# Kernel optimization log

Measured on AMD Instinct MI355X. Metric: run time of the kernel, lower is better.

Reference implementation:

```python
import jax, jax.numpy as jnp
import numpy as np

EMBED_DIM = 2048
NUM_HEADS = 32
NUM_KV_HEADS = 8
HEAD_DIM = EMBED_DIM // NUM_HEADS  # 64
KV_DIM = NUM_KV_HEADS * HEAD_DIM   # 512


def setup_inputs() -> dict:
    key = jax.random.key(0)
    ks = jax.random.split(key, 5)
    B, S = 2, 2048
    scale = 0.02
    x = jax.random.normal(ks[0], (B, S, EMBED_DIM), dtype=jnp.float32)
    Wq = jax.random.normal(ks[1], (EMBED_DIM, EMBED_DIM), dtype=jnp.float32) * scale
    Wk = jax.random.normal(ks[2], (EMBED_DIM, KV_DIM), dtype=jnp.float32) * scale
    Wv = jax.random.normal(ks[3], (EMBED_DIM, KV_DIM), dtype=jnp.float32) * scale
    Wo = jax.random.normal(ks[4], (EMBED_DIM, EMBED_DIM), dtype=jnp.float32) * scale
    return {"x": x, "Wq": Wq, "Wk": Wk, "Wv": Wv, "Wo": Wo}


def reference(x, Wq, Wk, Wv, Wo):
    B, S, _ = x.shape
    g = NUM_HEADS // NUM_KV_HEADS  # queries per kv head
    # projections -> [B, H, S, D]
    q = (x @ Wq).reshape(B, S, NUM_HEADS, HEAD_DIM).transpose(0, 2, 1, 3)
    k = (x @ Wk).reshape(B, S, NUM_KV_HEADS, HEAD_DIM).transpose(0, 2, 1, 3)
    v = (x @ Wv).reshape(B, S, NUM_KV_HEADS, HEAD_DIM).transpose(0, 2, 1, 3)
    # GQA repeat_interleave on head dim
    k = jnp.repeat(k, g, axis=1)
    v = jnp.repeat(v, g, axis=1)
    scores = jnp.einsum('bhqd,bhkd->bhqk', q, k) / np.sqrt(HEAD_DIM).astype(np.float32)
    causal = jnp.tril(jnp.ones((S, S), dtype=bool))
    scores = jnp.where(causal, scores, jnp.finfo(x.dtype).min)
    attn = jax.nn.softmax(scores, axis=-1)
    out = jnp.einsum('bhqk,bhkd->bhqd', attn, v)  # [B, H, S, D]
    out = out.transpose(0, 2, 1, 3).reshape(B, S, EMBED_DIM)
    return out @ Wo
```

## Files before the change

### kernel.cpp

```cpp
#include <hip/hip_runtime.h>
#include <hip/hip_bf16.h>
#include <cstdint>
#include <type_traits>

#define EMBED 2048
#define SLEN 2048
#define NB 2
#define NHEADS 32
#define HDIM 64
#define KVDIM 512
#define KVSTRIDE 1024
#define MTOT (NB * SLEN)
#define NQKV (EMBED + 2 * KVDIM)

typedef __attribute__((ext_vector_type(8))) __bf16 bf16x8;
typedef __attribute__((ext_vector_type(4))) float f32x4;
typedef __attribute__((ext_vector_type(16))) float f32x16;

#define QSCALE 0.18033688011112042f

__device__ __forceinline__ ushort f2bf(float f) {
    union { float f; uint32_t u; } v; v.f = f;
    uint32_t r = (v.u + 0x7FFFu + ((v.u >> 16) & 1u)) >> 16;
    return (ushort)r;
}

__device__ __forceinline__ void gload_lds16(const ushort* g, ushort* l) {
    __builtin_amdgcn_global_load_lds(
        (const __attribute__((address_space(1))) void*)g,
        (__attribute__((address_space(3))) void*)l, 16, 0, 0);
}

__global__ __launch_bounds__(256) void k_prep(const float* __restrict__ x,
                                              const float* __restrict__ Wq,
                                              const float* __restrict__ Wk,
                                              const float* __restrict__ Wv,
                                              const float* __restrict__ Wo,
                                              ushort* __restrict__ xb,
                                              ushort* __restrict__ wt,
                                              ushort* __restrict__ wot) {
    const int tid = threadIdx.x;
    int bid = blockIdx.x;
    if (bid < 8192) {
        int i = bid * 256 + tid;
        float4 v = *(const float4*)(x + (size_t)i * 4);
        ushort4 o;
        o.x = f2bf(v.x); o.y = f2bf(v.y); o.z = f2bf(v.z); o.w = f2bf(v.w);
        *(ushort4*)(xb + (size_t)i * 4) = o;
        return;
    }
    bid -= 8192;
    const float* W; ushort* Wt; int N; float scale; int bx, by;
    if (bid < 4096)      { W = Wq; Wt = wt;                                   N = EMBED; scale = QSCALE; bx = bid & 63; by = bid >> 6; }
    else if (bid < 5120) { W = Wk; Wt = wt + (size_t)EMBED * EMBED;           N = KVDIM; scale = 1.f; int b2 = bid - 4096; bx = b2 & 15; by = b2 >> 4; }
    else if (bid < 6144) { W = Wv; Wt = wt + (size_t)(EMBED + KVDIM) * EMBED; N = KVDIM; scale = 1.f; int b2 = bid - 5120; bx = b2 & 15; by = b2 >> 4; }
    else                 { W = Wo; Wt = wot;                                  N = EMBED; scale = 1.f; int b2 = bid - 6144; bx = b2 & 63; by = b2 >> 6; }
    const int K = EMBED;
    __shared__ float tile[32][33];
    const int tx = tid & 31, ty = tid >> 5;
    const int xcol = bx * 32 + tx;
    const int y0 = by * 32;
    #pragma unroll
    for (int i = ty; i < 32; i += 8)
        tile[i][tx] = W[(size_t)(y0 + i) * N + xcol];
    __syncthreads();
    const int xo = y0 + tx;
    const int yo0 = bx * 32;
    #pragma unroll
    for (int i = ty; i < 32; i += 8)
        Wt[(size_t)(yo0 + i) * K + xo] = f2bf(tile[tx][i] * scale);
}

__global__ __launch_bounds__(256) void k_transpose_v(const ushort* __restrict__ KV,
                                                     ushort* __restrict__ VT) {
    __shared__ ushort tile[64][65];
    const int tx = threadIdx.x, ty = threadIdx.y;
    const int x0 = blockIdx.x * 64;
    const int y0 = blockIdx.y * 64;
    #pragma unroll
    for (int i = ty; i < 64; i += 4)
        tile[i][tx] = KV[(size_t)(y0 + i) * KVSTRIDE + KVDIM + x0 + tx];
    __syncthreads();
    #pragma unroll
    for (int i = ty; i < 64; i += 4)
        VT[(size_t)(x0 + i) * MTOT + y0 + tx] = tile[tx][i];
}

__device__ __forceinline__ int2 xcd_swizzle(int gx, int gy) {
    const int nwg = gx * gy;
    int f = blockIdx.y * gx + blockIdx.x;
    const int cpx = nwg >> 3;
    f = (f & 7) * cpx + (f >> 3);
    return make_int2(f % gx, f / gx);
}

template <typename OUT_T>
__global__ __launch_bounds__(256) void k_gemm_bt(const ushort* __restrict__ A,
                                                 const ushort* __restrict__ Bt,
                                                 OUT_T* __restrict__ C,
                                                 int M, int N, int K) {
    __shared__ alignas(16) ushort As[2][128 * 64];
    __shared__ alignas(16) ushort Bs[2][128 * 64];

    const int tid = threadIdx.x;
    const int lane = tid & 63;
    const int w = tid >> 6;
    const int wr = w >> 1, wc = w & 1;
    const int l15 = lane & 15, g = lane >> 4;
    const int2 bxy = xcd_swizzle(N / 128, M / 128);
    const int n0 = bxy.x * 128;
    const int m0 = bxy.y * 128;

    f32x4 acc[4][4] = {};

    const ushort* pA[4];
    const ushort* pB[4];
    #pragma unroll
    for (int t = 0; t < 4; t++) {
        const int c = tid + 256 * t;
        const int r = c >> 3, gr = c & 7;
        const int sg = gr ^ (r & 7);
        pA[t] = A + (size_t)(m0 + r) * K + sg * 8;
        pB[t] = Bt + (size_t)(n0 + r) * K + sg * 8;
    }

    #pragma unroll
    for (int t = 0; t < 4; t++) {
        gload_lds16(pA[t], &As[0][(tid + 256 * t) * 8]);
        gload_lds16(pB[t], &Bs[0][(tid + 256 * t) * 8]);
    }
    __syncthreads();

    int cur = 0;
    for (int k0 = 0; k0 < K; k0 += 64) {
        if (k0 + 64 < K) {
            #pragma unroll
            for (int t = 0; t < 4; t++) {
                gload_lds16(pA[t] + k0 + 64, &As[cur ^ 1][(tid + 256 * t) * 8]);
                gload_lds16(pB[t] + k0 + 64, &Bs[cur ^ 1][(tid + 256 * t) * 8]);
            }
        }
        #pragma unroll
        for (int kk = 0; kk < 2; kk++) {
            bf16x8 a[4], b[4];
            #pragma unroll
            for (int i = 0; i < 4; i++)
                a[i] = *(const bf16x8*)&As[cur][(wr * 64 + i * 16 + l15) * 64 +
                                                (((4 * kk + g) ^ (l15 & 7)) << 3)];
            #pragma unroll
            for (int j = 0; j < 4; j++)
                b[j] = *(const bf16x8*)&Bs[cur][(wc * 64 + j * 16 + l15) * 64 +
                                                (((4 * kk + g) ^ (l15 & 7)) << 3)];
            #pragma unroll
            for (int i = 0; i < 4; i++)
                #pragma unroll
                for (int j = 0; j < 4; j++)
                    acc[i][j] = __builtin_amdgcn_mfma_f32_16x16x32_bf16(a[i], b[j], acc[i][j], 0, 0, 0);
        }
        __syncthreads();
        cur ^= 1;
    }

    #pragma unroll
    for (int i = 0; i < 4; i++) {
        #pragma unroll
        for (int j = 0; j < 4; j++) {
            const int row = m0 + wr * 64 + i * 16 + g * 4;
            const int col = n0 + wc * 64 + j * 16 + l15;
            #pragma unroll
            for (int r = 0; r < 4; r++) {
                float val = acc[i][j][r];
                if constexpr (std::is_same<OUT_T, ushort>::value)
                    C[(size_t)(row + r) * N + col] = f2bf(val);
                else
                    C[(size_t)(row + r) * N + col] = val;
            }
        }
    }
}

__global__ __launch_bounds__(256) void k_gemm_kv(const ushort* __restrict__ A,
                                                 const ushort* __restrict__ Bt,
                                                 ushort* __restrict__ C) {
    __shared__ alignas(16) ushort As[2][64 * 64];
    __shared__ alignas(16) ushort Bs[2][128 * 64];

    const int tid = threadIdx.x;
    const int lane = tid & 63;
    const int w = tid >> 6;
    const int wr = w >> 1, wc = w & 1;
    const int l15 = lane & 15, g = lane >> 4;
    const int2 bxy = xcd_swizzle(KVSTRIDE / 128, MTOT / 64);
    const int n0 = bxy.x * 128;
    const int m0 = bxy.y * 64;
    const int K = EMBED;

    f32x4 acc[2][4] = {};

    const ushort* pA[2];
    const ushort* pB[4];
    #pragma unroll
    for (int t = 0; t < 2; t++) {
        const int c = tid + 256 * t;
        const int r = c >> 3, gr = c & 7;
        const int sg = gr ^ (r & 7);
        pA[t] = A + (size_t)(m0 + r) * K + sg * 8;
    }
    #pragma unroll
    for (int t = 0; t < 4; t++) {
        const int c = tid + 256 * t;
        const int r = c >> 3, gr = c & 7;
        const int sg = gr ^ (r & 7);
        pB[t] = Bt + (size_t)(n0 + r) * K + sg * 8;
    }

    #pragma unroll
    for (int t = 0; t < 2; t++)
        gload_lds16(pA[t], &As[0][(tid + 256 * t) * 8]);
    #pragma unroll
    for (int t = 0; t < 4; t++)
        gload_lds16(pB[t], &Bs[0][(tid + 256 * t) * 8]);
    __syncthreads();

    int cur = 0;
    for (int k0 = 0; k0 < K; k0 += 64) {
        if (k0 + 64 < K) {
            #pragma unroll
            for (int t = 0; t < 2; t++)
                gload_lds16(pA[t] + k0 + 64, &As[cur ^ 1][(tid + 256 * t) * 8]);
            #pragma unroll
            for (int t = 0; t < 4; t++)
                gload_lds16(pB[t] + k0 + 64, &Bs[cur ^ 1][(tid + 256 * t) * 8]);
        }
        #pragma unroll
        for (int kk = 0; kk < 2; kk++) {
            bf16x8 a[2], b[4];
            #pragma unroll
            for (int i = 0; i < 2; i++)
                a[i] = *(const bf16x8*)&As[cur][(wr * 32 + i * 16 + l15) * 64 +
                                                (((4 * kk + g) ^ (l15 & 7)) << 3)];
            #pragma unroll
            for (int j = 0; j < 4; j++)
                b[j] = *(const bf16x8*)&Bs[cur][(wc * 64 + j * 16 + l15) * 64 +
                                                (((4 * kk + g) ^ (l15 & 7)) << 3)];
            #pragma unroll
            for (int i = 0; i < 2; i++)
                #pragma unroll
                for (int j = 0; j < 4; j++)
                    acc[i][j] = __builtin_amdgcn_mfma_f32_16x16x32_bf16(a[i], b[j], acc[i][j], 0, 0, 0);
        }
        __syncthreads();
        cur ^= 1;
    }

    #pragma unroll
    for (int i = 0; i < 2; i++) {
        #pragma unroll
        for (int j = 0; j < 4; j++) {
            const int row = m0 + wr * 32 + i * 16 + g * 4;
            const int col = n0 + wc * 64 + j * 16 + l15;
            #pragma unroll
            for (int r = 0; r < 4; r++)
                C[(size_t)(row + r) * KVSTRIDE + col] = f2bf(acc[i][j][r]);
        }
    }
}

__global__ __launch_bounds__(512, 4) void k_attn(const ushort* __restrict__ Qg,
                                                 const ushort* __restrict__ KVg,
                                                 const ushort* __restrict__ VTg,
                                                 ushort* __restrict__ Og) {
    __shared__ alignas(16) ushort Ks[2][64 * 64];
    __shared__ alignas(16) ushort Vs[2][64 * 64];

    const int tid = threadIdx.x;
    const int lane = tid & 63;
    const int wq = tid >> 6;
    const int l31 = lane & 31;
    const int hi = lane >> 5;

    const int flat = blockIdx.x + (blockIdx.y << 3) + (blockIdx.z << 8);
    const int lo = flat & 255, hv = flat >> 8;
    const int bi = hv ? (7 - (lo & 7)) : (lo & 7);
    const int h = lo >> 3;
    const int b = hv;
    const int kh = h >> 2;
    const size_t rowbase = (size_t)b * SLEN;

    const int q0 = bi * 256;
    const int qw0 = q0 + wq * 32;
    const int nt = (q0 >> 6) + 4;

    bf16x8 qf[4];
    {
        const ushort* qrow = Qg + (rowbase + qw0 + l31) * EMBED + h * HDIM;
        #pragma unroll
        for (int s = 0; s < 4; s++)
            qf[s] = *(const bf16x8*)(qrow + s * 16 + hi * 8);
    }

    const int srow = tid >> 3;
    const int sgr = tid & 7;
    const int woff = srow * 64 + ((sgr ^ (srow & 7)) << 3);
    const ushort* kgbase = KVg + (rowbase + srow) * KVSTRIDE + kh * HDIM + sgr * 8;
    const ushort* vgbase = VTg + (size_t)(kh * HDIM + srow) * MTOT + b * SLEN + sgr * 8;

    {
        uint4 kr = *(const uint4*)kgbase;
        uint4 vr = *(const uint4*)vgbase;
        *(uint4*)&Ks[0][woff] = kr;
        *(uint4*)&Vs[0][woff] = vr;
    }
    __syncthreads();

    f32x16 oacc[2];
    #pragma unroll
    for (int d = 0; d < 2; d++)
        #pragma unroll
        for (int r = 0; r < 16; r++) oacc[d][r] = 0.f;
    float l_run = 0.f;

    int cur = 0;
    for (int kt = 0; kt < nt; ++kt) {
        const int k0 = kt * 64;
        const bool pref = (kt + 1 < nt);
        uint4 kr, vr;
        if (pref) {
            kr = *(const uint4*)(kgbase + (size_t)(k0 + 64) * KVSTRIDE);
            vr = *(const uint4*)(vgbase + k0 + 64);
        }

        if (k0 <= qw0 + 31) {
            f32x16 sacc[2];
            #pragma unroll
            for (int st = 0; st < 2; st++)
                #pragma unroll
                for (int r = 0; r < 16; r++) sacc[st][r] = 0.f;
            __builtin_amdgcn_s_setprio(1);
            #pragma unroll
            for (int st = 0; st < 2; st++) {
                const int krow = st * 32 + l31;
                #pragma unroll
                for (int s = 0; s < 4; s++) {
                    bf16x8 af = *(const bf16x8*)&Ks[cur][krow * 64 + (((2 * s + hi) ^ (l31 & 7)) << 3)];
                    sacc[st] = __builtin_amdgcn_mfma_f32_32x32x16_bf16(af, qf[s], sacc[st], 0, 0, 0);
                }
            }
            __builtin_amdgcn_s_setprio(0);
            if (k0 + 63 > qw0) {
                const int q = qw0 + l31;
                #pragma unroll
                for (int st = 0; st < 2; st++)
                    #pragma unroll
                    for (int r = 0; r < 16; r++) {
                        int kpos = k0 + st * 32 + (r & 3) + 8 * (r >> 2) + 4 * hi;
                        if (kpos > q) sacc[st][r] = -1e30f;
                    }
            }
            float lsum = 0.f;
            #pragma unroll
            for (int st = 0; st < 2; st++)
                #pragma unroll
                for (int r = 0; r < 16; r++) {
                    float p = __builtin_amdgcn_exp2f(sacc[st][r]);
                    sacc[st][r] = p;
                    lsum += p;
                }
            lsum += __shfl_xor(lsum, 32);
            l_run += lsum;
            uint32_t pr[2][8];
            #pragma unroll
            for (int st = 0; st < 2; st++)
                #pragma unroll
                for (int k = 0; k < 8; k++) {
                    uint32_t d;
                    asm("v_cvt_pk_bf16_f32 %0, %1, %2"
                        : "=v"(d) : "v"(sacc[st][2 * k]), "v"(sacc[st][2 * k + 1]));
                    pr[st][k] = d;
                }
            #pragma unroll
            for (int c = 0; c < 2; c++) {
                #pragma unroll
                for (int tt = 0; tt < 2; tt++) {
                    const int pb = 4 * tt;
                    uint32_t w0 = pr[c][pb + 0], w2 = pr[c][pb + 2];
                    uint32_t w1 = pr[c][pb + 1], w3 = pr[c][pb + 3];
                    asm("v_permlane32_swap_b32 %0, %1" : "+v"(w0), "+v"(w2));
                    asm("v_permlane32_swap_b32 %0, %1" : "+v"(w1), "+v"(w3));
                    union { uint32_t u[4]; bf16x8 v; } pf;
                    pf.u[0] = w0; pf.u[1] = w1; pf.u[2] = w2; pf.u[3] = w3;
                    const int t = 2 * c + tt;
                    __builtin_amdgcn_s_setprio(1);
                    #pragma unroll
                    for (int dt = 0; dt < 2; dt++) {
                        const int vrow = dt * 32 + l31;
                        bf16x8 vf = *(const bf16x8*)&Vs[cur][vrow * 64 + (((2 * t + hi) ^ (l31 & 7)) << 3)];
                        oacc[dt] = __builtin_amdgcn_mfma_f32_32x32x16_bf16(pf.v, vf, oacc[dt], 0, 0, 0);
                    }
                    __builtin_amdgcn_s_setprio(0);
                }
            }
        }

        __syncthreads();
        if (pref) {
            *(uint4*)&Ks[cur ^ 1][woff] = kr;
            *(uint4*)&Vs[cur ^ 1][woff] = vr;
        }
        __syncthreads();
        cur ^= 1;
    }

    #pragma unroll
    for (int r = 0; r < 16; r++) {
        const int rr = (r & 3) + 8 * (r >> 2) + 4 * hi;
        float lr = __shfl(l_run, rr | (lane & 32));
        float inv = 1.f / lr;
        const size_t base = (rowbase + qw0 + rr) * EMBED + h * HDIM;
        Og[base + l31] = f2bf(oacc[0][r] * inv);
        Og[base + 32 + l31] = f2bf(oacc[1][r] * inv);
    }
}

#define WS_XB  ((size_t)0)
#define WS_QB  (WS_XB + (size_t)MTOT * EMBED)
#define WS_KVB (WS_QB + (size_t)MTOT * EMBED)
#define WS_WT  (WS_KVB + (size_t)MTOT * KVSTRIDE)
#define WS_WOT (WS_WT + (size_t)NQKV * EMBED)
#define WS_VT  WS_WT

extern "C" void kernel_launch(void* const* d_in, const int* in_sizes, int n_in,
                              void* d_out, int out_size, void* d_ws, size_t ws_size,
                              hipStream_t stream) {
    const float* x  = (const float*)d_in[0];
    const float* Wq = (const float*)d_in[1];
    const float* Wk = (const float*)d_in[2];
    const float* Wv = (const float*)d_in[3];
    const float* Wo = (const float*)d_in[4];
    float* out = (float*)d_out;
    ushort* ws = (ushort*)d_ws;

    k_prep<<<18432, 256, 0, stream>>>(x, Wq, Wk, Wv, Wo,
                                      ws + WS_XB, ws + WS_WT, ws + WS_WOT);

    k_gemm_bt<ushort><<<dim3(EMBED / 128, MTOT / 128), 256, 0, stream>>>(
        ws + WS_XB, ws + WS_WT, ws + WS_QB, MTOT, EMBED, EMBED);

    k_gemm_kv<<<dim3(KVSTRIDE / 128, MTOT / 64), 256, 0, stream>>>(
        ws + WS_XB, ws + WS_WT + (size_t)EMBED * EMBED, ws + WS_KVB);

    k_transpose_v<<<dim3(KVDIM / 64, MTOT / 64), dim3(64, 4), 0, stream>>>(
        ws + WS_KVB, ws + WS_VT);

    k_attn<<<dim3(8, 32, 2), 512, 0, stream>>>(
        ws + WS_QB, ws + WS_KVB, ws + WS_VT, ws + WS_XB);

    k_gemm_bt<float><<<dim3(EMBED / 128, MTOT / 128), 256, 0, stream>>>(
        ws + WS_XB, ws + WS_WOT, out, MTOT, EMBED, EMBED);
}
```

Measured before the change: 191.2 us.

## Merge Q and KV projection GEMMs into one launch; compute softmax row sums via MFMA

Combines the separate Q projection and KV projection GEMM kernels into a single launch of 1024 blocks, where the first 512 blocks do Q tiles and the rest do KV tiles. This removes one kernel launch and lets the two GEMMs share the machine instead of running back to back. In attention, the per-row softmax denominator is now accumulated by an extra MFMA against a ones vector instead of scalar adds plus a cross-lane shuffle. That costs additional MFMA work and 16 more accumulator registers per thread, which may pressure occupancy.

```diff
diff --git a/kernel.cpp b/kernel.cpp
--- a/kernel.cpp
+++ b/kernel.cpp
@@ -86,12 +86,157 @@
         VT[(size_t)(x0 + i) * MTOT + y0 + tx] = tile[tx][i];
 }
 
-__device__ __forceinline__ int2 xcd_swizzle(int gx, int gy) {
-    const int nwg = gx * gy;
-    int f = blockIdx.y * gx + blockIdx.x;
-    const int cpx = nwg >> 3;
-    f = (f & 7) * cpx + (f >> 3);
-    return make_int2(f % gx, f / gx);
+__global__ __launch_bounds__(256) void k_gemm_qkv2(const ushort* __restrict__ A,
+                                                   const ushort* __restrict__ WtAll,
+                                                   ushort* __restrict__ Qb,
+                                                   ushort* __restrict__ KVb) {
+    __shared__ alignas(16) ushort As[2][128 * 64];
+    __shared__ alignas(16) ushort Bs[2][128 * 64];
+
+    const int tid = threadIdx.x;
+    const int lane = tid & 63;
+    const int w = tid >> 6;
+    const int wr = w >> 1, wc = w & 1;
+    const int l15 = lane & 15, g = lane >> 4;
+    const int K = EMBED;
+    const int bid = blockIdx.x;
+
+    if (bid < 512) {
+        int f = (bid & 7) * 64 + (bid >> 3);
+        const int bx = f % (EMBED / 128), by = f / (EMBED / 128);
+        const int n0 = bx * 128, m0 = by * 128;
+        const ushort* Bt = WtAll;
+
+        f32x4 acc[4][4] = {};
+        const ushort* pA[4];
+        const ushort* pB[4];
+        #pragma unroll
+        for (int t = 0; t < 4; t++) {
+            const int c = tid + 256 * t;
+            const int r = c >> 3, gr = c & 7;
+            const int sg = gr ^ (r & 7);
+            pA[t] = A + (size_t)(m0 + r) * K + sg * 8;
+            pB[t] = Bt + (size_t)(n0 + r) * K + sg * 8;
+        }
+        #pragma unroll
+        for (int t = 0; t < 4; t++) {
+            gload_lds16(pA[t], &As[0][(tid + 256 * t) * 8]);
+            gload_lds16(pB[t], &Bs[0][(tid + 256 * t) * 8]);
+        }
+        __syncthreads();
+
+        int cur = 0;
+        for (int k0 = 0; k0 < K; k0 += 64) {
+            if (k0 + 64 < K) {
+                #pragma unroll
+                for (int t = 0; t < 4; t++) {
+                    gload_lds16(pA[t] + k0 + 64, &As[cur ^ 1][(tid + 256 * t) * 8]);
+                    gload_lds16(pB[t] + k0 + 64, &Bs[cur ^ 1][(tid + 256 * t) * 8]);
+                }
+            }
+            #pragma unroll
+            for (int kk = 0; kk < 2; kk++) {
+                bf16x8 a[4], b[4];
+                #pragma unroll
+                for (int i = 0; i < 4; i++)
+                    a[i] = *(const bf16x8*)&As[cur][(wr * 64 + i * 16 + l15) * 64 +
+                                                    (((4 * kk + g) ^ (l15 & 7)) << 3)];
+                #pragma unroll
+                for (int j = 0; j < 4; j++)
+                    b[j] = *(const bf16x8*)&Bs[cur][(wc * 64 + j * 16 + l15) * 64 +
+                                                    (((4 * kk + g) ^ (l15 & 7)) << 3)];
+                #pragma unroll
+                for (int i = 0; i < 4; i++)
+                    #pragma unroll
+                    for (int j = 0; j < 4; j++)
+                        acc[i][j] = __builtin_amdgcn_mfma_f32_16x16x32_bf16(a[i], b[j], acc[i][j], 0, 0, 0);
+            }
+            __syncthreads();
+            cur ^= 1;
+        }
+        #pragma unroll
+        for (int i = 0; i < 4; i++)
+            #pragma unroll
+            for (int j = 0; j < 4; j++) {
+                const int row = m0 + wr * 64 + i * 16 + g * 4;
+                const int col = n0 + wc * 64 + j * 16 + l15;
+                #pragma unroll
+                for (int r = 0; r < 4; r++)
+                    Qb[(size_t)(row + r) * EMBED + col] = f2bf(acc[i][j][r]);
+            }
+    } else {
+        int f0 = bid - 512;
+        int f = (f0 & 7) * 64 + (f0 >> 3);
+        const int bx = f % (KVSTRIDE / 128), by = f / (KVSTRIDE / 128);
+        const int n0 = bx * 128, m0 = by * 64;
+        const ushort* Bt = WtAll + (size_t)EMBED * EMBED;
+
+        f32x4 acc[2][4] = {};
+        const ushort* pA[2];
+        const ushort* pB[4];
+        #pragma unroll
+        for (int t = 0; t < 2; t++) {
+            const int c = tid + 256 * t;
+            const int r = c >> 3, gr = c & 7;
+            const int sg = gr ^ (r & 7);
+            pA[t] = A + (size_t)(m0 + r) * K + sg * 8;
+        }
+        #pragma unroll
+        for (int t = 0; t < 4; t++) {
+            const int c = tid + 256 * t;
+            const int r = c >> 3, gr = c & 7;
+            const int sg = gr ^ (r & 7);
+            pB[t] = Bt + (size_t)(n0 + r) * K + sg * 8;
+        }
+        #pragma unroll
+        for (int t = 0; t < 2; t++)
+            gload_lds16(pA[t], &As[0][(tid + 256 * t) * 8]);
+        #pragma unroll
+        for (int t = 0; t < 4; t++)
+            gload_lds16(pB[t], &Bs[0][(tid + 256 * t) * 8]);
+        __syncthreads();
+
+        int cur = 0;
+        for (int k0 = 0; k0 < K; k0 += 64) {
+            if (k0 + 64 < K) {
+                #pragma unroll
+                for (int t = 0; t < 2; t++)
+                    gload_lds16(pA[t] + k0 + 64, &As[cur ^ 1][(tid + 256 * t) * 8]);
+                #pragma unroll
+                for (int t = 0; t < 4; t++)
+                    gload_lds16(pB[t] + k0 + 64, &Bs[cur ^ 1][(tid + 256 * t) * 8]);
+            }
+            #pragma unroll
+            for (int kk = 0; kk < 2; kk++) {
+                bf16x8 a[2], b[4];
+                #pragma unroll
+                for (int i = 0; i < 2; i++)
+                    a[i] = *(const bf16x8*)&As[cur][(wr * 32 + i * 16 + l15) * 64 +
+                                                    (((4 * kk + g) ^ (l15 & 7)) << 3)];
+                #pragma unroll
+                for (int j = 0; j < 4; j++)
+                    b[j] = *(const bf16x8*)&Bs[cur][(wc * 64 + j * 16 + l15) * 64 +
+                                                    (((4 * kk + g) ^ (l15 & 7)) << 3)];
+                #pragma unroll
+                for (int i = 0; i < 2; i++)
+                    #pragma unroll
+                    for (int j = 0; j < 4; j++)
+                        acc[i][j] = __builtin_amdgcn_mfma_f32_16x16x32_bf16(a[i], b[j], acc[i][j], 0, 0, 0);
+            }
+            __syncthreads();
+            cur ^= 1;
+        }
+        #pragma unroll
+        for (int i = 0; i < 2; i++)
+            #pragma unroll
+            for (int j = 0; j < 4; j++) {
+                const int row = m0 + wr * 32 + i * 16 + g * 4;
+                const int col = n0 + wc * 64 + j * 16 + l15;
+                #pragma unroll
+                for (int r = 0; r < 4; r++)
+                    KVb[(size_t)(row + r) * KVSTRIDE + col] = f2bf(acc[i][j][r]);
+            }
+    }
 }
 
 template <typename OUT_T>
@@ -107,9 +252,11 @@
     const int w = tid >> 6;
     const int wr = w >> 1, wc = w & 1;
     const int l15 = lane & 15, g = lane >> 4;
-    const int2 bxy = xcd_swizzle(N / 128, M / 128);
-    const int n0 = bxy.x * 128;
-    const int m0 = bxy.y * 128;
+    const int nwg = (N / 128) * (M / 128);
+    int f = blockIdx.y * (N / 128) + blockIdx.x;
+    f = (f & 7) * (nwg >> 3) + (f >> 3);
+    const int n0 = (f % (N / 128)) * 128;
+    const int m0 = (f / (N / 128)) * 128;
 
     f32x4 acc[4][4] = {};
 
@@ -175,93 +322,6 @@
                 else
                     C[(size_t)(row + r) * N + col] = val;
             }
-        }
-    }
-}
-
-__global__ __launch_bounds__(256) void k_gemm_kv(const ushort* __restrict__ A,
-                                                 const ushort* __restrict__ Bt,
-                                                 ushort* __restrict__ C) {
-    __shared__ alignas(16) ushort As[2][64 * 64];
-    __shared__ alignas(16) ushort Bs[2][128 * 64];
-
-    const int tid = threadIdx.x;
-    const int lane = tid & 63;
-    const int w = tid >> 6;
-    const int wr = w >> 1, wc = w & 1;
-    const int l15 = lane & 15, g = lane >> 4;
-    const int2 bxy = xcd_swizzle(KVSTRIDE / 128, MTOT / 64);
-    const int n0 = bxy.x * 128;
-    const int m0 = bxy.y * 64;
-    const int K = EMBED;
-
-    f32x4 acc[2][4] = {};
-
-    const ushort* pA[2];
-    const ushort* pB[4];
-    #pragma unroll
-    for (int t = 0; t < 2; t++) {
-        const int c = tid + 256 * t;
-        const int r = c >> 3, gr = c & 7;
-        const int sg = gr ^ (r & 7);
-        pA[t] = A + (size_t)(m0 + r) * K + sg * 8;
-    }
-    #pragma unroll
-    for (int t = 0; t < 4; t++) {
-        const int c = tid + 256 * t;
-        const int r = c >> 3, gr = c & 7;
-        const int sg = gr ^ (r & 7);
-        pB[t] = Bt + (size_t)(n0 + r) * K + sg * 8;
-    }
-
-    #pragma unroll
-    for (int t = 0; t < 2; t++)
-        gload_lds16(pA[t], &As[0][(tid + 256 * t) * 8]);
-    #pragma unroll
-    for (int t = 0; t < 4; t++)
-        gload_lds16(pB[t], &Bs[0][(tid + 256 * t) * 8]);
-    __syncthreads();
-
-    int cur = 0;
-    for (int k0 = 0; k0 < K; k0 += 64) {
-        if (k0 + 64 < K) {
-            #pragma unroll
-            for (int t = 0; t < 2; t++)
-                gload_lds16(pA[t] + k0 + 64, &As[cur ^ 1][(tid + 256 * t) * 8]);
-            #pragma unroll
-            for (int t = 0; t < 4; t++)
-                gload_lds16(pB[t] + k0 + 64, &Bs[cur ^ 1][(tid + 256 * t) * 8]);
-        }
-        #pragma unroll
-        for (int kk = 0; kk < 2; kk++) {
-            bf16x8 a[2], b[4];
-            #pragma unroll
-            for (int i = 0; i < 2; i++)
-                a[i] = *(const bf16x8*)&As[cur][(wr * 32 + i * 16 + l15) * 64 +
-                                                (((4 * kk + g) ^ (l15 & 7)) << 3)];
-            #pragma unroll
-            for (int j = 0; j < 4; j++)
-                b[j] = *(const bf16x8*)&Bs[cur][(wc * 64 + j * 16 + l15) * 64 +
-                                                (((4 * kk + g) ^ (l15 & 7)) << 3)];
-            #pragma unroll
-            for (int i = 0; i < 2; i++)
-                #pragma unroll
-                for (int j = 0; j < 4; j++)
-                    acc[i][j] = __builtin_amdgcn_mfma_f32_16x16x32_bf16(a[i], b[j], acc[i][j], 0, 0, 0);
-        }
-        __syncthreads();
-        cur ^= 1;
-    }
-
-    #pragma unroll
-    for (int i = 0; i < 2; i++) {
-        #pragma unroll
-        for (int j = 0; j < 4; j++) {
-            const int row = m0 + wr * 32 + i * 16 + g * 4;
-            const int col = n0 + wc * 64 + j * 16 + l15;
-            #pragma unroll
-            for (int r = 0; r < 4; r++)
-                C[(size_t)(row + r) * KVSTRIDE + col] = f2bf(acc[i][j][r]);
         }
     }
 }
@@ -299,6 +359,10 @@
             qf[s] = *(const bf16x8*)(qrow + s * 16 + hi * 8);
     }
 
+    union { uint32_t u[4]; bf16x8 v; } onesf;
+    onesf.u[0] = 0x3F803F80u; onesf.u[1] = 0x3F803F80u;
+    onesf.u[2] = 0x3F803F80u; onesf.u[3] = 0x3F803F80u;
+
     const int srow = tid >> 3;
     const int sgr = tid & 7;
     const int woff = srow * 64 + ((sgr ^ (srow & 7)) << 3);
@@ -313,12 +377,13 @@
     }
     __syncthreads();
 
-    f32x16 oacc[2];
+    f32x16 oacc[2], lacc;
     #pragma unroll
     for (int d = 0; d < 2; d++)
         #pragma unroll
         for (int r = 0; r < 16; r++) oacc[d][r] = 0.f;
-    float l_run = 0.f;
+    #pragma unroll
+    for (int r = 0; r < 16; r++) lacc[r] = 0.f;
 
     int cur = 0;
     for (int kt = 0; kt < nt; ++kt) {
@@ -357,17 +422,11 @@
                         if (kpos > q) sacc[st][r] = -1e30f;
                     }
             }
-            float lsum = 0.f;
             #pragma unroll
             for (int st = 0; st < 2; st++)
                 #pragma unroll
-                for (int r = 0; r < 16; r++) {
-                    float p = __builtin_amdgcn_exp2f(sacc[st][r]);
-                    sacc[st][r] = p;
-                    lsum += p;
-                }
-            lsum += __shfl_xor(lsum, 32);
-            l_run += lsum;
+                for (int r = 0; r < 16; r++)
+                    sacc[st][r] = __builtin_amdgcn_exp2f(sacc[st][r]);
             uint32_t pr[2][8];
             #pragma unroll
             for (int st = 0; st < 2; st++)
@@ -391,6 +450,7 @@
                     pf.u[0] = w0; pf.u[1] = w1; pf.u[2] = w2; pf.u[3] = w3;
                     const int t = 2 * c + tt;
                     __builtin_amdgcn_s_setprio(1);
+                    lacc = __builtin_amdgcn_mfma_f32_32x32x16_bf16(pf.v, onesf.v, lacc, 0, 0, 0);
                     #pragma unroll
                     for (int dt = 0; dt < 2; dt++) {
                         const int vrow = dt * 32 + l31;
@@ -414,8 +474,7 @@
     #pragma unroll
     for (int r = 0; r < 16; r++) {
         const int rr = (r & 3) + 8 * (r >> 2) + 4 * hi;
-        float lr = __shfl(l_run, rr | (lane & 32));
-        float inv = 1.f / lr;
+        float inv = 1.f / lacc[r];
         const size_t base = (rowbase + qw0 + rr) * EMBED + h * HDIM;
         Og[base + l31] = f2bf(oacc[0][r] * inv);
         Og[base + 32 + l31] = f2bf(oacc[1][r] * inv);
@@ -443,11 +502,8 @@
     k_prep<<<18432, 256, 0, stream>>>(x, Wq, Wk, Wv, Wo,
                                       ws + WS_XB, ws + WS_WT, ws + WS_WOT);
 
-    k_gemm_bt<ushort><<<dim3(EMBED / 128, MTOT / 128), 256, 0, stream>>>(
-        ws + WS_XB, ws + WS_WT, ws + WS_QB, MTOT, EMBED, EMBED);
-
-    k_gemm_kv<<<dim3(KVSTRIDE / 128, MTOT / 64), 256, 0, stream>>>(
-        ws + WS_XB, ws + WS_WT + (size_t)EMBED * EMBED, ws + WS_KVB);
+    k_gemm_qkv2<<<1024, 256, 0, stream>>>(
+        ws + WS_XB, ws + WS_WT, ws + WS_QB, ws + WS_KVB);
 
     k_transpose_v<<<dim3(KVDIM / 64, MTOT / 64), dim3(64, 4), 0, stream>>>(
         ws + WS_KVB, ws + WS_VT);
```

Result: no change. 188.2 us (-1.6%).
